# Kernel optimization log

Hardware: AMD Instinct MI355X
Metric: run time of the kernel (lower is better)

Reference implementation:

```python
import jax, jax.numpy as jnp
import numpy as np

PC = (-51.2, -51.2, -5.0, 51.2, 51.2, 3.0)
BEV_H, BEV_W, BEV_Z = 50, 50, 4
NCAM, NUM_HEADS = 6, 8
EPS = 1e-5


def _layer_norm(x, g, b):
    m = jnp.mean(x, -1, keepdims=True)
    v = jnp.mean((x - m) ** 2, -1, keepdims=True)
    return (x - m) / jnp.sqrt(v + 1e-5) * g + b


def _grid_sample(imgs, pts):
    # imgs: (B,C,H,W); pts: (B,N,2) normalized coords; bilinear,
    # align_corners=False, zero padding (matches F.grid_sample defaults).
    B, C, H, W = imgs.shape
    def one(img, p):
        x = ((p[:, 0] + 1.0) * W - 1.0) * 0.5
        y = ((p[:, 1] + 1.0) * H - 1.0) * 0.5
        x0 = jnp.floor(x); y0 = jnp.floor(y)
        wx = x - x0; wy = y - y0
        def g(xi, yi):
            ok = (xi >= 0) & (xi < W) & (yi >= 0) & (yi < H)
            v = img[:, jnp.clip(yi, 0, H - 1).astype(jnp.int32),
                       jnp.clip(xi, 0, W - 1).astype(jnp.int32)]
            return v * ok[None, :]
        return (g(x0, y0) * (1 - wx) * (1 - wy) + g(x0 + 1, y0) * wx * (1 - wy)
                + g(x0, y0 + 1) * (1 - wx) * wy + g(x0 + 1, y0 + 1) * wx * wy)
    return jax.vmap(one)(imgs, pts)  # (B,C,N)


def _mha(q, kv, inW, inb, outW, outb):
    # torch nn.MultiheadAttention (batch_first)
    C = q.shape[-1]; d = C // NUM_HEADS
    B, Nq = q.shape[:2]; Nk = kv.shape[1]
    Q = q @ inW[:C].T + inb[:C]
    K = kv @ inW[C:2 * C].T + inb[C:2 * C]
    V = kv @ inW[2 * C:].T + inb[2 * C:]
    Qh = Q.reshape(B, Nq, NUM_HEADS, d).transpose(0, 2, 1, 3)
    Kh = K.reshape(B, Nk, NUM_HEADS, d).transpose(0, 2, 1, 3)
    Vh = V.reshape(B, Nk, NUM_HEADS, d).transpose(0, 2, 1, 3)
    s = jnp.einsum('bhqd,bhkd->bhqk', Qh, Kh) / float(np.sqrt(d))
    a = jax.nn.softmax(s, axis=-1)
    o = jnp.einsum('bhqk,bhkd->bhqd', a, Vh).transpose(0, 2, 1, 3).reshape(B, Nq, C)
    return o @ outW.T + outb


def _warp_prev(prev_bev, ego_motion):
    B, N, C = prev_bev.shape
    sp = prev_bev.transpose(0, 2, 1).reshape(B, C, BEV_H, BEV_W)
    tx = ego_motion[:, 0, 3]; ty = ego_motion[:, 1, 3]
    yaw = jnp.arctan2(ego_motion[:, 1, 0], ego_motion[:, 0, 0])
    dx = tx / ((PC[3] - PC[0]) / BEV_W) * 2.0 / BEV_W
    dy = ty / ((PC[4] - PC[1]) / BEV_H) * 2.0 / BEV_H
    c = jnp.cos(yaw); s = jnp.sin(yaw)
    theta = jnp.stack([jnp.stack([c, -s, dx], -1),
                       jnp.stack([s, c, dy], -1)], axis=1)  # (B,2,3)
    # F.affine_grid, align_corners=False: output-pixel-center base grid
    xs = (2.0 * jnp.arange(BEV_W) + 1.0) / BEV_W - 1.0
    ys = (2.0 * jnp.arange(BEV_H) + 1.0) / BEV_H - 1.0
    gx, gy = jnp.meshgrid(xs, ys)  # (H,W) each
    base = jnp.stack([gx, gy, jnp.ones_like(gx)], -1)  # (H,W,3)
    grid = jnp.einsum('bij,hwj->bhwi', theta, base).reshape(B, -1, 2)
    out = _grid_sample(sp, grid)  # (B,C,N)
    return out.transpose(0, 2, 1)


def _reference_points(B):
    ys = (jnp.arange(BEV_H, dtype=jnp.float32) + 0.5) / BEV_H
    xs = (jnp.arange(BEV_W, dtype=jnp.float32) + 0.5) / BEV_W
    ry, rx = jnp.meshgrid(ys, xs, indexing='ij')
    rx = rx.reshape(-1); ry = ry.reshape(-1)
    zs = (jnp.arange(BEV_Z, dtype=jnp.float32) + 0.5) / BEV_Z
    N = BEV_H * BEV_W
    ref = jnp.stack([jnp.broadcast_to(rx[:, None], (N, BEV_Z)),
                     jnp.broadcast_to(ry[:, None], (N, BEV_Z)),
                     jnp.broadcast_to(zs[None, :], (N, BEV_Z))], -1)
    return jnp.broadcast_to(ref[None], (B, N, BEV_Z, 3))  # (B,Nq,Z,3)


def _point_sampling(ref, img_feats, lidar2img):
    B, Nq, Zb, _ = ref.shape
    _, Ncam, C, Hf, Wf = img_feats.shape
    x = ref[..., 0] * (PC[3] - PC[0]) + PC[0]
    y = ref[..., 1] * (PC[4] - PC[1]) + PC[1]
    z = ref[..., 2] * (PC[5] - PC[2]) + PC[2]
    pts = jnp.stack([x, y, z, jnp.ones_like(x)], -1).reshape(B, 1, Nq * Zb, 4)
    pts = jnp.broadcast_to(pts, (B, Ncam, Nq * Zb, 4))
    cam = jnp.einsum('bnij,bnpj->bnpi', lidar2img, pts)
    depth = cam[..., 2]
    xy = cam[..., 0:2] / jnp.clip(depth, EPS)[..., None]
    gx = (xy[..., 0] / (Wf - 1) - 0.5) * 2.0
    gy = (xy[..., 1] / (Hf - 1) - 0.5) * 2.0
    valid = ((depth > EPS) & (gx > -1.0) & (gx < 1.0)
             & (gy > -1.0) & (gy < 1.0))  # (B,Ncam,Nq*Zb)
    grid = jnp.stack([gx, gy], -1).reshape(B * Ncam, Nq * Zb, 2)
    samp = _grid_sample(img_feats.reshape(B * Ncam, C, Hf, Wf), grid)
    samp = samp.reshape(B, Ncam, C, Nq, Zb) * valid.reshape(B, Ncam, 1, Nq, Zb)
    return jnp.nan_to_num(samp)


def _forward(query, prev_bev, img_feats, ego_motion, lidar2img,
             attn_w_W, attn_w_b, sca_out_W, sca_out_b,
             in_proj_W, in_proj_b, mha_out_W, mha_out_b,
             norm1_g, norm1_b, ffn_W1, ffn_b1, ffn_W2, ffn_b2,
             norm2_g, norm2_b):
    B, Nq, C = query.shape
    # Temporal self-attention with warped previous BEV
    aligned = _warp_prev(prev_bev, ego_motion)
    kv = jnp.concatenate([query, aligned], axis=1)
    attn = _mha(query, kv, in_proj_W, in_proj_b, mha_out_W, mha_out_b)
    q = _layer_norm(query + attn, norm1_g, norm1_b)
    # Spatial cross attention
    ref = _reference_points(B)
    samp = _point_sampling(ref, img_feats, lidar2img)  # (B,Ncam,C,Nq,Z)
    w = (q @ attn_w_W.T + attn_w_b).reshape(B, Nq, NCAM * BEV_Z)
    w = jax.nn.softmax(w, axis=-1).reshape(B, Nq, NCAM, BEV_Z)
    agg = jnp.einsum('bncqz,bqnz->bqc', samp, w)
    q = agg @ sca_out_W.T + sca_out_b + q
    # FFN (Linear -> ReLU -> Linear -> LayerNorm), residual outside
    h = jax.nn.relu(q @ ffn_W1.T + ffn_b1) @ ffn_W2.T + ffn_b2
    return q + _layer_norm(h, norm2_g, norm2_b)


def setup_inputs() -> dict:
    key = jax.random.key(0)
    ks = jax.random.split(key, 16)
    B, Nq, C, Hf, Wf = 1, BEV_H * BEV_W, 256, 28, 50
    s = 0.02
    d = {
        'query': jax.random.normal(ks[0], (B, Nq, C), jnp.float32),
        'prev_bev': jax.random.normal(ks[1], (B, Nq, C), jnp.float32),
        'img_feats': jax.random.normal(ks[2], (B, NCAM, C, Hf, Wf), jnp.float32),
        'ego_motion': jax.random.normal(ks[3], (B, 4, 4), jnp.float32),
        'lidar2img': jax.random.normal(ks[4], (B, NCAM, 4, 4), jnp.float32),
        'attn_w_W': jax.random.normal(ks[5], (NCAM * BEV_Z, C), jnp.float32) * s,
        'attn_w_b': jnp.zeros((NCAM * BEV_Z,), jnp.float32),
        'sca_out_W': jax.random.normal(ks[6], (C, C), jnp.float32) * s,
        'sca_out_b': jnp.zeros((C,), jnp.float32),
        'in_proj_W': jax.random.normal(ks[7], (3 * C, C), jnp.float32) * s,
        'in_proj_b': jnp.zeros((3 * C,), jnp.float32),
        'mha_out_W': jax.random.normal(ks[8], (C, C), jnp.float32) * s,
        'mha_out_b': jnp.zeros((C,), jnp.float32),
        'norm1_g': jnp.ones((C,), jnp.float32),
        'norm1_b': jnp.zeros((C,), jnp.float32),
        'ffn_W1': jax.random.normal(ks[9], (2 * C, C), jnp.float32) * s,
        'ffn_b1': jnp.zeros((2 * C,), jnp.float32),
        'ffn_W2': jax.random.normal(ks[10], (C, 2 * C), jnp.float32) * s,
        'ffn_b2': jnp.zeros((C,), jnp.float32),
        'norm2_g': jnp.ones((C,), jnp.float32),
        'norm2_b': jnp.zeros((C,), jnp.float32),
    }
    return d


def reference(query, prev_bev, img_feats, ego_motion, lidar2img,
              attn_w_W, attn_w_b, sca_out_W, sca_out_b,
              in_proj_W, in_proj_b, mha_out_W, mha_out_b,
              norm1_g, norm1_b, ffn_W1, ffn_b1, ffn_W2, ffn_b2,
              norm2_g, norm2_b):
    return _forward(query, prev_bev, img_feats, ego_motion, lidar2img,
                    attn_w_W, attn_w_b, sca_out_W, sca_out_b,
                    in_proj_W, in_proj_b, mha_out_W, mha_out_b,
                    norm1_g, norm1_b, ffn_W1, ffn_b1, ffn_W2, ffn_b2,
                    norm2_g, norm2_b)
```

## Files before the change

### kernel.cpp

```cpp
#include <hip/hip_runtime.h>
#include <hip/hip_bf16.h>
#include <math.h>

#define NQ   2500
#define CDIM 256
#define NKV  5000
#define NH   8
#define DH   32
#define SPLITS 10
#define KPS   500
#define FULLT 7
#define TAILNK 52

typedef __attribute__((ext_vector_type(8))) short bf16x8;
typedef __attribute__((ext_vector_type(4))) short short4v;
typedef __attribute__((ext_vector_type(4))) float f32x4;

#define MFMA __builtin_amdgcn_mfma_f32_16x16x32_bf16

__device__ __forceinline__ short f2bf(float f) {
  union { float f; unsigned u; } v; v.f = f;
  unsigned r = v.u + 0x7FFFu + ((v.u >> 16) & 1u);
  return (short)(r >> 16);
}
__device__ __forceinline__ float bf2f(unsigned short s) {
  union { unsigned u; float f; } x; x.u = ((unsigned)s) << 16; return x.f;
}
__device__ __forceinline__ unsigned pk_trunc(float a, float b) {
  union { float f; unsigned u; } x, y; x.f = a; y.f = b;
  return (y.u & 0xFFFF0000u) | (x.u >> 16);
}
__device__ __forceinline__ unsigned cvt_pk_bf16(float a, float b) {
  unsigned r;
  asm("v_cvt_pk_bf16_f32 %0, %1, %2" : "=v"(r) : "v"(a), "v"(b));
  return r;
}
__device__ __forceinline__ float exp2_fast(float x) {
  float r; asm("v_exp_f32 %0, %1" : "=v"(r) : "v"(x)); return r;
}
__device__ __forceinline__ bf16x8 cat4(short4v a, short4v b) {
  bf16x8 r;
  r[0]=a[0]; r[1]=a[1]; r[2]=a[2]; r[3]=a[3];
  r[4]=b[0]; r[5]=b[1]; r[6]=b[2]; r[7]=b[3];
  return r;
}

__global__ __launch_bounds__(256) void k_build_kv(
    const float* __restrict__ query, const float* __restrict__ prev,
    const float* __restrict__ ego, float* __restrict__ kv)
{
  int row = blockIdx.x, c = threadIdx.x;
  if (row < NQ) { kv[(size_t)row*CDIM + c] = query[(size_t)row*CDIM + c]; return; }
  int n = row - NQ;
  float txm = ego[3], tym = ego[7];
  float yaw = atan2f(ego[4], ego[0]);
  float cs = cosf(yaw), sn = sinf(yaw);
  float dx = txm * (1.f/51.2f), dy = tym * (1.f/51.2f);
  int i = n / 50, j = n % 50;
  float gx = (2.f*j + 1.f)*(1.f/50.f) - 1.f;
  float gy = (2.f*i + 1.f)*(1.f/50.f) - 1.f;
  float px = cs*gx - sn*gy + dx;
  float py = sn*gx + cs*gy + dy;
  float xf = ((px + 1.f)*50.f - 1.f)*0.5f;
  float yf = ((py + 1.f)*50.f - 1.f)*0.5f;
  float x0f = floorf(xf), y0f = floorf(yf);
  int x0 = (int)x0f, y0 = (int)y0f;
  float wx = xf - x0f, wy = yf - y0f;
  float v00 = (x0  >=0 && x0  <50 && y0  >=0 && y0  <50) ? prev[((size_t)(y0*50+x0      ))*CDIM + c] : 0.f;
  float v10 = (x0+1>=0 && x0+1<50 && y0  >=0 && y0  <50) ? prev[((size_t)(y0*50+x0+1    ))*CDIM + c] : 0.f;
  float v01 = (x0  >=0 && x0  <50 && y0+1>=0 && y0+1<50) ? prev[((size_t)((y0+1)*50+x0  ))*CDIM + c] : 0.f;
  float v11 = (x0+1>=0 && x0+1<50 && y0+1>=0 && y0+1<50) ? prev[((size_t)((y0+1)*50+x0+1))*CDIM + c] : 0.f;
  float v = (v00*(1.f-wx) + v10*wx)*(1.f-wy) + (v01*(1.f-wx) + v11*wx)*wy;
  kv[(size_t)row*CDIM + c] = v;
}

__global__ __launch_bounds__(256) void k_transpose_img(
    const float* __restrict__ img, unsigned short* __restrict__ imgT)
{
  int b = blockIdx.x;
  int n = b / 28, y = b % 28;
  int c = threadIdx.x;
  for (int x = 0; x < 50; ++x)
    imgT[((size_t)((n*28 + y)*50 + x))*CDIM + c] =
      (unsigned short)f2bf(img[((size_t)(n*CDIM + c)*28 + y)*50 + x]);
}

__global__ __launch_bounds__(256) void k_gemm(
    const float* __restrict__ A, const float* __restrict__ W,
    const float* __restrict__ bias, const float* __restrict__ res,
    float* __restrict__ C, short* __restrict__ Cb,
    int M, int N, int K, int relu, int mode, float scale)
{
  __shared__ short Abf[8][33][8];
  __shared__ short Wbf[8][65][8];
  const int tid = threadIdx.x;
  const int lane = tid & 63, wid = tid >> 6;
  const int wm = wid >> 1, wn = wid & 1;
  const int g = lane >> 4, c = lane & 15;
  const int m0 = blockIdx.y << 5, n0 = blockIdx.x << 6;
  const int srow = tid >> 3, skq = tid & 7;
  f32x4 acc0 = {0.f,0.f,0.f,0.f}, acc1 = acc0;
  const float4 z4 = make_float4(0.f,0.f,0.f,0.f);
  for (int k0 = 0; k0 < K; k0 += 64) {
    float4 fa0 = z4, fa1 = z4;
    if (m0 + srow < M) {
      const float* ap = A + (size_t)(m0+srow)*K + k0 + skq*8;
      fa0 = *(const float4*)ap; fa1 = *(const float4*)(ap+4);
    }
    const float* wp0 = W + (size_t)(n0+srow)*K + k0 + skq*8;
    const float* wp1 = W + (size_t)(n0+32+srow)*K + k0 + skq*8;
    const float4 fw00 = *(const float4*)wp0, fw01 = *(const float4*)(wp0+4);
    const float4 fw10 = *(const float4*)wp1, fw11 = *(const float4*)(wp1+4);
    __syncthreads();
    union { unsigned u[4]; bf16x8 v; } pa, pw0, pw1;
    pa.u[0]  = cvt_pk_bf16(fa0.x, fa0.y);  pa.u[1]  = cvt_pk_bf16(fa0.z, fa0.w);
    pa.u[2]  = cvt_pk_bf16(fa1.x, fa1.y);  pa.u[3]  = cvt_pk_bf16(fa1.z, fa1.w);
    pw0.u[0] = cvt_pk_bf16(fw00.x, fw00.y); pw0.u[1] = cvt_pk_bf16(fw00.z, fw00.w);
    pw0.u[2] = cvt_pk_bf16(fw01.x, fw01.y); pw0.u[3] = cvt_pk_bf16(fw01.z, fw01.w);
    pw1.u[0] = cvt_pk_bf16(fw10.x, fw10.y); pw1.u[1] = cvt_pk_bf16(fw10.z, fw10.w);
    pw1.u[2] = cvt_pk_bf16(fw11.x, fw11.y); pw1.u[3] = cvt_pk_bf16(fw11.z, fw11.w);
    *(bf16x8*)&Abf[skq][srow][0]      = pa.v;
    *(bf16x8*)&Wbf[skq][srow][0]      = pw0.v;
    *(bf16x8*)&Wbf[skq][32+srow][0]   = pw1.v;
    __syncthreads();
    #pragma unroll
    for (int s = 0; s < 2; ++s) {
      const bf16x8 fA  = *(const bf16x8*)&Abf[s*4+g][wm*16 + c][0];
      const bf16x8 fW0 = *(const bf16x8*)&Wbf[s*4+g][wn*32 + c][0];
      const bf16x8 fW1 = *(const bf16x8*)&Wbf[s*4+g][wn*32 + 16 + c][0];
      acc0 = MFMA(fA, fW0, acc0, 0,0,0);
      acc1 = MFMA(fA, fW1, acc1, 0,0,0);
    }
  }
  const int nc0 = n0 + wn*32 + c, nc1 = nc0 + 16;
  const float b0v = bias[nc0], b1v = bias[nc1];
  #pragma unroll
  for (int r = 0; r < 4; ++r) {
    const int m = m0 + wm*16 + g*4 + r;
    if (m >= M) continue;
    float v0 = acc0[r] + b0v;
    float v1 = acc1[r] + b1v;
    if (mode == 0) {
      if (res) { v0 += res[(size_t)m*N + nc0]; v1 += res[(size_t)m*N + nc1]; }
      if (relu) { v0 = fmaxf(v0, 0.f); v1 = fmaxf(v1, 0.f); }
      C[(size_t)m*N + nc0] = v0;
      C[(size_t)m*N + nc1] = v1;
    } else if (mode == 1) {
      Cb[(size_t)m*N + nc0] = f2bf(v0*scale);
      Cb[(size_t)m*N + nc1] = f2bf(v1*scale);
    } else {
      Cb[(size_t)nc0*M + m] = f2bf(v0);
      Cb[(size_t)nc1*M + m] = f2bf(v1);
    }
  }
}

__device__ __forceinline__ void softmax_pv(
    f32x4 s0, f32x4 s1, f32x4 s2, f32x4 s3, bool tail, int g,
    float& m, float& l, f32x4& oA, f32x4& oB,
    bf16x8 A0lo, bf16x8 A0hi, bf16x8 A1lo, bf16x8 A1hi)
{
  float sv[16];
  #pragma unroll
  for (int r=0;r<4;++r){ sv[r]=s0[r]; sv[4+r]=s1[r]; sv[8+r]=s2[r]; sv[12+r]=s3[r]; }
  if (tail) {
    #pragma unroll
    for (int i=0;i<16;++i) {
      const int kl = (i>>2)*16 + g*4 + (i&3);
      if (kl >= TAILNK) sv[i] = -1e30f;
    }
  }
  float mx = fmaxf(fmaxf(fmaxf(sv[0],sv[1]),fmaxf(sv[2],sv[3])),
                   fmaxf(fmaxf(sv[4],sv[5]),fmaxf(sv[6],sv[7])));
  mx = fmaxf(mx, fmaxf(fmaxf(fmaxf(sv[8],sv[9]),fmaxf(sv[10],sv[11])),
                       fmaxf(fmaxf(sv[12],sv[13]),fmaxf(sv[14],sv[15]))));
  if (!__all(mx <= m + 8.f)) {
    float mm = fmaxf(mx, __shfl_xor(mx, 16));
    mm = fmaxf(mm, __shfl_xor(mm, 32));
    const float mn = fmaxf(m, mm);
    const float scl = exp2_fast(m - mn);
    m = mn;
    l *= scl;
    #pragma unroll
    for (int r=0;r<4;++r){ oA[r]*=scl; oB[r]*=scl; }
  }
  float p[16]; float ps = 0.f;
  #pragma unroll
  for (int i=0;i<16;++i){ p[i] = exp2_fast(sv[i]-m); ps += p[i]; }
  l += ps;
  union { unsigned u[4]; bf16x8 v; } b0, b1;
  #pragma unroll
  for (int i=0;i<4;++i) {
    b0.u[i] = pk_trunc(p[2*i],   p[2*i+1]);
    b1.u[i] = pk_trunc(p[8+2*i], p[8+2*i+1]);
  }
  oA = MFMA(A0lo, b0.v, oA, 0,0,0);
  oA = MFMA(A0hi, b1.v, oA, 0,0,0);
  oB = MFMA(A1lo, b0.v, oB, 0,0,0);
  oB = MFMA(A1hi, b1.v, oB, 0,0,0);
}

__global__ __launch_bounds__(64) void k_flash4(
    const short* __restrict__ Qbf, const short* __restrict__ Kbf,
    const short* __restrict__ VbfT, short* __restrict__ opart,
    float* __restrict__ mlp)
{
  const int lane = threadIdx.x;
  const int g = lane >> 4, c = lane & 15;
  const int h = blockIdx.y, sp = blockIdx.z;
  const int q0 = blockIdx.x * 32;
  const int qa  = min(q0 +      c, NQ-1);
  const int qb2 = min(q0 + 16 + c, NQ-1);
  const bf16x8 qf0 = *(const bf16x8*)(Qbf + (size_t)qa *CDIM + h*DH + g*8);
  const bf16x8 qf1 = *(const bf16x8*)(Qbf + (size_t)qb2*CDIM + h*DH + g*8);
  const int kbase = sp*KPS;
  const size_t doff = (size_t)h*DH + g*8;
  const short* kbp = Kbf + (size_t)(kbase + c)*CDIM + doff;
  const short* vr0 = VbfT + (size_t)(h*DH +      c)*NKV + kbase;
  const short* vr1 = VbfT + (size_t)(h*DH + 16 + c)*NKV + kbase;
  const f32x4 z = {0.f,0.f,0.f,0.f};
  f32x4 o00 = z, o01 = z, o10 = z, o11 = z;
  float m0v = -INFINITY, l0 = 0.f, m1v = -INFINITY, l1 = 0.f;

  bf16x8 kc0 = *(const bf16x8*)(kbp);
  bf16x8 kc1 = *(const bf16x8*)(kbp + (size_t)16*CDIM);
  bf16x8 kc2 = *(const bf16x8*)(kbp + (size_t)32*CDIM);
  bf16x8 kc3 = *(const bf16x8*)(kbp + (size_t)48*CDIM);

  #pragma unroll
  for (int t = 0; t < FULLT; ++t) {
    const int kt = t*64;
    const f32x4 s00 = MFMA(kc0, qf0, z, 0,0,0);
    const f32x4 s01 = MFMA(kc1, qf0, z, 0,0,0);
    const f32x4 s02 = MFMA(kc2, qf0, z, 0,0,0);
    const f32x4 s03 = MFMA(kc3, qf0, z, 0,0,0);
    const f32x4 s10 = MFMA(kc0, qf1, z, 0,0,0);
    const f32x4 s11 = MFMA(kc1, qf1, z, 0,0,0);
    const f32x4 s12 = MFMA(kc2, qf1, z, 0,0,0);
    const f32x4 s13 = MFMA(kc3, qf1, z, 0,0,0);
    if (t+1 < FULLT) {
      kc0 = *(const bf16x8*)(kbp + (size_t)(kt+64)*CDIM);
      kc1 = *(const bf16x8*)(kbp + (size_t)(kt+80)*CDIM);
      kc2 = *(const bf16x8*)(kbp + (size_t)(kt+96)*CDIM);
      kc3 = *(const bf16x8*)(kbp + (size_t)(kt+112)*CDIM);
    }
    const short4v x00 = *(const short4v*)(vr0 + kt      + g*4);
    const short4v x01 = *(const short4v*)(vr0 + kt + 16 + g*4);
    const short4v x02 = *(const short4v*)(vr0 + kt + 32 + g*4);
    const short4v x03 = *(const short4v*)(vr0 + kt + 48 + g*4);
    const short4v x10 = *(const short4v*)(vr1 + kt      + g*4);
    const short4v x11 = *(const short4v*)(vr1 + kt + 16 + g*4);
    const short4v x12 = *(const short4v*)(vr1 + kt + 32 + g*4);
    const short4v x13 = *(const short4v*)(vr1 + kt + 48 + g*4);
    const bf16x8 A0lo = cat4(x00, x01), A0hi = cat4(x02, x03);
    const bf16x8 A1lo = cat4(x10, x11), A1hi = cat4(x12, x13);
    softmax_pv(s00,s01,s02,s03, false, g, m0v, l0, o00, o01, A0lo, A0hi, A1lo, A1hi);
    softmax_pv(s10,s11,s12,s13, false, g, m1v, l1, o10, o11, A0lo, A0hi, A1lo, A1hi);
  }
  {
    const int kt = FULLT*64;
    const int ka0 = min(kbase + kt +      c, NKV-1);
    const int ka1 = min(kbase + kt + 16 + c, NKV-1);
    const int ka2 = min(kbase + kt + 32 + c, NKV-1);
    const int ka3 = min(kbase + kt + 48 + c, NKV-1);
    const bf16x8 kf0 = *(const bf16x8*)(Kbf + (size_t)ka0*CDIM + doff);
    const bf16x8 kf1 = *(const bf16x8*)(Kbf + (size_t)ka1*CDIM + doff);
    const bf16x8 kf2 = *(const bf16x8*)(Kbf + (size_t)ka2*CDIM + doff);
    const bf16x8 kf3 = *(const bf16x8*)(Kbf + (size_t)ka3*CDIM + doff);
    const f32x4 s00 = MFMA(kf0, qf0, z, 0,0,0);
    const f32x4 s01 = MFMA(kf1, qf0, z, 0,0,0);
    const f32x4 s02 = MFMA(kf2, qf0, z, 0,0,0);
    const f32x4 s03 = MFMA(kf3, qf0, z, 0,0,0);
    const f32x4 s10 = MFMA(kf0, qf1, z, 0,0,0);
    const f32x4 s11 = MFMA(kf1, qf1, z, 0,0,0);
    const f32x4 s12 = MFMA(kf2, qf1, z, 0,0,0);
    const f32x4 s13 = MFMA(kf3, qf1, z, 0,0,0);
    const int o0 = min(kt      + g*4, KPS-4);
    const int o1 = min(kt + 16 + g*4, KPS-4);
    const int o2 = min(kt + 32 + g*4, KPS-4);
    const int o3 = min(kt + 48 + g*4, KPS-4);
    const short4v x00 = *(const short4v*)(vr0 + o0);
    const short4v x01 = *(const short4v*)(vr0 + o1);
    const short4v x02 = *(const short4v*)(vr0 + o2);
    const short4v x03 = *(const short4v*)(vr0 + o3);
    const short4v x10 = *(const short4v*)(vr1 + o0);
    const short4v x11 = *(const short4v*)(vr1 + o1);
    const short4v x12 = *(const short4v*)(vr1 + o2);
    const short4v x13 = *(const short4v*)(vr1 + o3);
    const bf16x8 A0lo = cat4(x00, x01), A0hi = cat4(x02, x03);
    const bf16x8 A1lo = cat4(x10, x11), A1hi = cat4(x12, x13);
    softmax_pv(s00,s01,s02,s03, true, g, m0v, l0, o00, o01, A0lo, A0hi, A1lo, A1hi);
    softmax_pv(s10,s11,s12,s13, true, g, m1v, l1, o10, o11, A0lo, A0hi, A1lo, A1hi);
  }
  l0 += __shfl_xor(l0, 16); l0 += __shfl_xor(l0, 32);
  l1 += __shfl_xor(l1, 16); l1 += __shfl_xor(l1, 32);

  const size_t ob0 = (size_t)(sp*NH + h)*NQ;
  const int qw0 = q0 + c;
  if (qw0 < NQ) {
    const size_t b = (ob0 + qw0)*DH;
    #pragma unroll
    for (int r=0;r<4;++r) {
      opart[b +      g*4 + r] = f2bf(o00[r]);
      opart[b + 16 + g*4 + r] = f2bf(o01[r]);
    }
    if (g == 0) { mlp[(ob0 + qw0)*2] = m0v; mlp[(ob0 + qw0)*2+1] = l0; }
  }
  const int qw1 = q0 + 16 + c;
  if (qw1 < NQ) {
    const size_t b = (ob0 + qw1)*DH;
    #pragma unroll
    for (int r=0;r<4;++r) {
      opart[b +      g*4 + r] = f2bf(o10[r]);
      opart[b + 16 + g*4 + r] = f2bf(o11[r]);
    }
    if (g == 0) { mlp[(ob0 + qw1)*2] = m1v; mlp[(ob0 + qw1)*2+1] = l1; }
  }
}

__global__ __launch_bounds__(256) void k_combine(
    const short* __restrict__ opart, const float* __restrict__ mlp,
    float* __restrict__ attn)
{
  const int q = blockIdx.x, t = threadIdx.x;
  const int h = t >> 5, d = t & 31;
  float ms[SPLITS], ls[SPLITS];
  float mstar = -INFINITY;
  #pragma unroll
  for (int s = 0; s < SPLITS; ++s) {
    size_t b = (size_t)(s*NH + h)*NQ + q;
    ms[s] = mlp[b*2]; ls[s] = mlp[b*2+1];
    mstar = fmaxf(mstar, ms[s]);
  }
  float num = 0.f, den = 0.f;
  #pragma unroll
  for (int s = 0; s < SPLITS; ++s) {
    float e = exp2_fast(ms[s] - mstar);
    size_t b = (size_t)(s*NH + h)*NQ + q;
    num += bf2f((unsigned short)opart[b*DH + d])*e;
    den += ls[s]*e;
  }
  attn[(size_t)q*CDIM + t] = num/den;
}

__global__ __launch_bounds__(256) void k_ln(
    const float* __restrict__ x, const float* __restrict__ g,
    const float* __restrict__ b, const float* __restrict__ post_res,
    float* __restrict__ out)
{
  const int row = blockIdx.x, c = threadIdx.x;
  const size_t idx = (size_t)row*CDIM + c;
  const float v = x[idx];
  __shared__ float red[4];
  float s = v;
  #pragma unroll
  for (int m = 1; m < 64; m <<= 1) s += __shfl_xor(s, m);
  if ((c & 63) == 0) red[c >> 6] = s;
  __syncthreads();
  const float mean = (red[0]+red[1]+red[2]+red[3]) * (1.f/256.f);
  const float dv = v - mean;
  __syncthreads();
  float s2 = dv*dv;
  #pragma unroll
  for (int m = 1; m < 64; m <<= 1) s2 += __shfl_xor(s2, m);
  if ((c & 63) == 0) red[c >> 6] = s2;
  __syncthreads();
  const float var = (red[0]+red[1]+red[2]+red[3]) * (1.f/256.f);
  float o = dv * rsqrtf(var + 1e-5f) * g[c] + b[c];
  if (post_res) o += post_res[idx];
  out[idx] = o;
}

__global__ __launch_bounds__(256) void k_sample_agg(
    const float* __restrict__ q1, const unsigned short* __restrict__ imgT,
    const float* __restrict__ l2i, const float* __restrict__ awW,
    const float* __restrict__ awb, float* __restrict__ agg)
{
  const int q = blockIdx.x, tid = threadIdx.x;
  __shared__ float qrow[256];
  __shared__ float wl[24];
  __shared__ float fwx[24], fwy[24];
  __shared__ int iv[24], ix[24], iy[24];
  qrow[tid] = q1[(size_t)q*CDIM + tid];
  __syncthreads();
  if (tid < 192) {
    const int e = tid >> 3, s2 = tid & 7;
    float acc = 0.f;
    for (int c = s2; c < 256; c += 8) acc += qrow[c]*awW[e*256 + c];
    acc += __shfl_xor(acc,1);
    acc += __shfl_xor(acc,2);
    acc += __shfl_xor(acc,4);
    if (s2 == 0) wl[e] = acc + awb[e];
  }
  if (tid < 24) {
    const int e = tid, n = e >> 2, z = e & 3;
    const int iyq = q / 50, jxq = q % 50;
    const float rx = (jxq + 0.5f)*(1.f/50.f);
    const float ry = (iyq + 0.5f)*(1.f/50.f);
    const float rz = (z + 0.5f)*0.25f;
    const float X = rx*102.4f - 51.2f;
    const float Y = ry*102.4f - 51.2f;
    const float Z = rz*8.f - 5.f;
    const float* L = l2i + n*16;
    const float cx = L[0]*X + L[1]*Y + L[2]*Z  + L[3];
    const float cy = L[4]*X + L[5]*Y + L[6]*Z  + L[7];
    const float cd = L[8]*X + L[9]*Y + L[10]*Z + L[11];
    const float dn = fmaxf(cd, 1e-5f);
    const float u = cx/dn, vv = cy/dn;
    const float gx = (u*(1.f/49.f) - 0.5f)*2.f;
    const float gy = (vv*(1.f/27.f) - 0.5f)*2.f;
    const int ok = (cd > 1e-5f) && (gx > -1.f) && (gx < 1.f) && (gy > -1.f) && (gy < 1.f);
    const float xf = ((gx + 1.f)*50.f - 1.f)*0.5f;
    const float yf = ((gy + 1.f)*28.f - 1.f)*0.5f;
    const float x0f = floorf(xf), y0f = floorf(yf);
    iv[e] = ok; ix[e] = (int)x0f; iy[e] = (int)y0f;
    fwx[e] = xf - x0f; fwy[e] = yf - y0f;
  }
  __syncthreads();
  float mx = -INFINITY;
  #pragma unroll
  for (int e = 0; e < 24; ++e) mx = fmaxf(mx, wl[e]);
  float se = 0.f;
  #pragma unroll
  for (int e = 0; e < 24; ++e) se += __expf(wl[e]-mx);
  const float inv = 1.f/se;
  const int c = tid;
  float acc = 0.f;
  #pragma unroll
  for (int e = 0; e < 24; ++e) {
    if (!iv[e]) continue;
    const float w = __expf(wl[e]-mx)*inv;
    const int n = e >> 2;
    const int x0 = ix[e], y0 = iy[e];
    const float wx = fwx[e], wy = fwy[e];
    const size_t base = (size_t)(n*28)*50;
    float v00 = (x0  >=0 && x0  <50 && y0  >=0 && y0  <28) ? bf2f(imgT[((base + (size_t)y0*50     + x0  ))*CDIM + c]) : 0.f;
    float v10 = (x0+1>=0 && x0+1<50 && y0  >=0 && y0  <28) ? bf2f(imgT[((base + (size_t)y0*50     + x0+1))*CDIM + c]) : 0.f;
    float v01 = (x0  >=0 && x0  <50 && y0+1>=0 && y0+1<28) ? bf2f(imgT[((base + (size_t)(y0+1)*50 + x0  ))*CDIM + c]) : 0.f;
    float v11 = (x0+1>=0 && x0+1<50 && y0+1>=0 && y0+1<28) ? bf2f(imgT[((base + (size_t)(y0+1)*50 + x0+1))*CDIM + c]) : 0.f;
    acc += w * ((v00*(1.f-wx) + v10*wx)*(1.f-wy) + (v01*(1.f-wx) + v11*wx)*wy);
  }
  agg[(size_t)q*CDIM + c] = acc;
}

extern "C" void kernel_launch(void* const* d_in, const int* in_sizes, int n_in,
                              void* d_out, int out_size, void* d_ws, size_t ws_size,
                              hipStream_t stream)
{
  const float* query = (const float*)d_in[0];
  const float* prev  = (const float*)d_in[1];
  const float* img   = (const float*)d_in[2];
  const float* ego   = (const float*)d_in[3];
  const float* l2i   = (const float*)d_in[4];
  const float* awW   = (const float*)d_in[5];
  const float* awb   = (const float*)d_in[6];
  const float* scaW  = (const float*)d_in[7];
  const float* scab  = (const float*)d_in[8];
  const float* inW   = (const float*)d_in[9];
  const float* inb   = (const float*)d_in[10];
  const float* moW   = (const float*)d_in[11];
  const float* mob   = (const float*)d_in[12];
  const float* n1g   = (const float*)d_in[13];
  const float* n1b   = (const float*)d_in[14];
  const float* fW1   = (const float*)d_in[15];
  const float* fb1   = (const float*)d_in[16];
  const float* fW2   = (const float*)d_in[17];
  const float* fb2   = (const float*)d_in[18];
  const float* n2g   = (const float*)d_in[19];
  const float* n2b   = (const float*)d_in[20];
  float* out = (float*)d_out;
  float* ws  = (float*)d_ws;

  float* kv    = ws;
  short* Qbf   = (short*)(ws + 1280000);
  short* Kbf   = (short*)(ws + 1600000);
  short* VbfT  = (short*)(ws + 2240000);
  short* opart = (short*)(ws + 2880000);
  float* mlp   = ws + 6080000;
  unsigned short* imgT = (unsigned short*)(ws + 6480000);
  float* attn  = ws;
  float* tmp1  = ws +  640000;
  float* q1    = ws + 1280000;
  float* aggb  = ws + 1920000;
  float* q2    = ws + 2560000;
  float* hbuf  = ws + 3200000;
  float* h2    = ws + 4480000;

  const float qscale = 0.2550727452794943f;

  k_build_kv<<<NKV, 256, 0, stream>>>(query, prev, ego, kv);
  k_transpose_img<<<6*28, 256, 0, stream>>>(img, imgT);
  k_gemm<<<dim3(4,79),  256, 0, stream>>>(kv, inW,          inb,     nullptr, nullptr, Qbf,  NQ,  256, 256, 0, 1, qscale);
  k_gemm<<<dim3(4,157), 256, 0, stream>>>(kv, inW + 65536,  inb+256, nullptr, nullptr, Kbf,  NKV, 256, 256, 0, 1, 1.0f);
  k_gemm<<<dim3(4,157), 256, 0, stream>>>(kv, inW + 131072, inb+512, nullptr, nullptr, VbfT, NKV, 256, 256, 0, 2, 1.0f);
  k_flash4<<<dim3(79, NH, SPLITS), 64, 0, stream>>>(Qbf, Kbf, VbfT, opart, mlp);
  k_combine<<<NQ, 256, 0, stream>>>(opart, mlp, attn);
  k_gemm<<<dim3(4,79), 256, 0, stream>>>(attn, moW, mob, query, tmp1, nullptr, NQ, 256, 256, 0, 0, 1.0f);
  k_ln<<<NQ, 256, 0, stream>>>(tmp1, n1g, n1b, nullptr, q1);
  k_sample_agg<<<NQ, 256, 0, stream>>>(q1, imgT, l2i, awW, awb, aggb);
  k_gemm<<<dim3(4,79), 256, 0, stream>>>(aggb, scaW, scab, q1, q2, nullptr, NQ, 256, 256, 0, 0, 1.0f);
  k_gemm<<<dim3(8,79), 256, 0, stream>>>(q2, fW1, fb1, nullptr, hbuf, nullptr, NQ, 512, 256, 1, 0, 1.0f);
  k_gemm<<<dim3(4,79), 256, 0, stream>>>(hbuf, fW2, fb2, nullptr, h2, nullptr, NQ, 256, 512, 0, 0, 1.0f);
  k_ln<<<NQ, 256, 0, stream>>>(h2, n2g, n2b, q2, out);
}
```

Baseline: 149.7 us.

## Prepack weights and V into MFMA fragment layout, flatten flash grid

Adds a per-call kernel that converts all projection and FFN weights to bf16 in MFMA fragment order, so the GEMM reads B fragments straight from global memory instead of converting and staging them through shared memory. Adds a repack kernel that rearranges V into per-tile fragment order, letting the flash kernel load each operand with one 16-byte load instead of gathering short4 pieces. The flash grid is flattened so that heads and splits of the same query block are launched next to each other. Two extra launches and more workspace traffic are the price.

```diff
diff --git a/kernel.cpp b/kernel.cpp
--- a/kernel.cpp
+++ b/kernel.cpp
@@ -10,6 +10,7 @@
 #define SPLITS 10
 #define KPS   500
 #define FULLT 7
+#define TILES 8
 #define TAILNK 52
 
 typedef __attribute__((ext_vector_type(8))) short bf16x8;
@@ -37,12 +38,6 @@
 }
 __device__ __forceinline__ float exp2_fast(float x) {
   float r; asm("v_exp_f32 %0, %1" : "=v"(r) : "v"(x)); return r;
-}
-__device__ __forceinline__ bf16x8 cat4(short4v a, short4v b) {
-  bf16x8 r;
-  r[0]=a[0]; r[1]=a[1]; r[2]=a[2]; r[3]=a[3];
-  r[4]=b[0]; r[5]=b[1]; r[6]=b[2]; r[7]=b[3];
-  return r;
 }
 
 __global__ __launch_bounds__(256) void k_build_kv(
@@ -74,6 +69,51 @@
   kv[(size_t)row*CDIM + c] = v;
 }
 
+__global__ __launch_bounds__(256) void k_prep_w(
+    const float* __restrict__ inW, const float* __restrict__ moW,
+    const float* __restrict__ scaW, const float* __restrict__ fW1,
+    const float* __restrict__ fW2, short* __restrict__ wf)
+{
+  const int id = blockIdx.x*256 + threadIdx.x;
+  if (id >= 73728) return;
+  const int s = id*8;
+  const float* src; int off, K, obase;
+  if      (s < 65536)  { src = inW;          off = s;          K = 256; obase = 0; }
+  else if (s < 131072) { src = inW + 65536;  off = s - 65536;  K = 256; obase = 65536; }
+  else if (s < 196608) { src = inW + 131072; off = s - 131072; K = 256; obase = 131072; }
+  else if (s < 262144) { src = moW;          off = s - 196608; K = 256; obase = 196608; }
+  else if (s < 327680) { src = scaW;         off = s - 262144; K = 256; obase = 262144; }
+  else if (s < 458752) { src = fW1;          off = s - 327680; K = 256; obase = 327680; }
+  else                 { src = fW2;          off = s - 458752; K = 512; obase = 458752; }
+  const int n = off / K, k = off - n*K;
+  short4v lo, hi;
+  #pragma unroll
+  for (int j = 0; j < 4; ++j) { lo[j] = f2bf(src[off+j]); hi[j] = f2bf(src[off+4+j]); }
+  short* dst = wf + obase + (size_t)((n>>4)*(K>>3) + (k>>3))*128 + (n&15)*8;
+  *(short4v*)dst = lo;
+  *(short4v*)(dst+4) = hi;
+}
+
+__global__ __launch_bounds__(256) void k_repack_v(
+    const short* __restrict__ VbfT, short* __restrict__ Vf)
+{
+  const int idx = blockIdx.x*256 + threadIdx.x;
+  const int j    = idx & 7;
+  const int lane = (idx >> 3) & 63;
+  const int i    = (idx >> 9) & 1;
+  const int kt2  = (idx >> 10) & 1;
+  const int t    = (idx >> 11) & 7;
+  const int h    = (idx >> 14) & 7;
+  const int sp   = idx >> 17;
+  const int gg = lane >> 4, cc = lane & 15;
+  const int ko32 = ((j >> 2) << 4) | (gg << 2) | (j & 3);
+  const int kin = t*64 + kt2*32 + ko32;
+  const int d = i*16 + cc;
+  short v = 0;
+  if (kin < KPS) v = VbfT[(size_t)(h*32 + d)*NKV + sp*KPS + kin];
+  Vf[idx] = v;
+}
+
 __global__ __launch_bounds__(256) void k_transpose_img(
     const float* __restrict__ img, unsigned short* __restrict__ imgT)
 {
@@ -86,19 +126,21 @@
 }
 
 __global__ __launch_bounds__(256) void k_gemm(
-    const float* __restrict__ A, const float* __restrict__ W,
+    const float* __restrict__ A, const short* __restrict__ Wf,
     const float* __restrict__ bias, const float* __restrict__ res,
     float* __restrict__ C, short* __restrict__ Cb,
     int M, int N, int K, int relu, int mode, float scale)
 {
   __shared__ short Abf[8][33][8];
-  __shared__ short Wbf[8][65][8];
   const int tid = threadIdx.x;
   const int lane = tid & 63, wid = tid >> 6;
   const int wm = wid >> 1, wn = wid & 1;
   const int g = lane >> 4, c = lane & 15;
   const int m0 = blockIdx.y << 5, n0 = blockIdx.x << 6;
   const int srow = tid >> 3, skq = tid & 7;
+  const int kb8 = K >> 3;
+  const short* wfa = Wf + (size_t)((n0 + wn*32) >> 4)      * kb8 * 128 + c*8;
+  const short* wfb = Wf + (size_t)(((n0 + wn*32) >> 4) + 1) * kb8 * 128 + c*8;
   f32x4 acc0 = {0.f,0.f,0.f,0.f}, acc1 = acc0;
   const float4 z4 = make_float4(0.f,0.f,0.f,0.f);
   for (int k0 = 0; k0 < K; k0 += 64) {
@@ -107,27 +149,18 @@
       const float* ap = A + (size_t)(m0+srow)*K + k0 + skq*8;
       fa0 = *(const float4*)ap; fa1 = *(const float4*)(ap+4);
     }
-    const float* wp0 = W + (size_t)(n0+srow)*K + k0 + skq*8;
-    const float* wp1 = W + (size_t)(n0+32+srow)*K + k0 + skq*8;
-    const float4 fw00 = *(const float4*)wp0, fw01 = *(const float4*)(wp0+4);
-    const float4 fw10 = *(const float4*)wp1, fw11 = *(const float4*)(wp1+4);
     __syncthreads();
-    union { unsigned u[4]; bf16x8 v; } pa, pw0, pw1;
-    pa.u[0]  = cvt_pk_bf16(fa0.x, fa0.y);  pa.u[1]  = cvt_pk_bf16(fa0.z, fa0.w);
-    pa.u[2]  = cvt_pk_bf16(fa1.x, fa1.y);  pa.u[3]  = cvt_pk_bf16(fa1.z, fa1.w);
-    pw0.u[0] = cvt_pk_bf16(fw00.x, fw00.y); pw0.u[1] = cvt_pk_bf16(fw00.z, fw00.w);
-    pw0.u[2] = cvt_pk_bf16(fw01.x, fw01.y); pw0.u[3] = cvt_pk_bf16(fw01.z, fw01.w);
-    pw1.u[0] = cvt_pk_bf16(fw10.x, fw10.y); pw1.u[1] = cvt_pk_bf16(fw10.z, fw10.w);
-    pw1.u[2] = cvt_pk_bf16(fw11.x, fw11.y); pw1.u[3] = cvt_pk_bf16(fw11.z, fw11.w);
-    *(bf16x8*)&Abf[skq][srow][0]      = pa.v;
-    *(bf16x8*)&Wbf[skq][srow][0]      = pw0.v;
-    *(bf16x8*)&Wbf[skq][32+srow][0]   = pw1.v;
+    union { unsigned u[4]; bf16x8 v; } pa;
+    pa.u[0] = cvt_pk_bf16(fa0.x, fa0.y);  pa.u[1] = cvt_pk_bf16(fa0.z, fa0.w);
+    pa.u[2] = cvt_pk_bf16(fa1.x, fa1.y);  pa.u[3] = cvt_pk_bf16(fa1.z, fa1.w);
+    *(bf16x8*)&Abf[skq][srow][0] = pa.v;
     __syncthreads();
     #pragma unroll
     for (int s = 0; s < 2; ++s) {
+      const int kq = (k0 >> 3) + s*4 + g;
       const bf16x8 fA  = *(const bf16x8*)&Abf[s*4+g][wm*16 + c][0];
-      const bf16x8 fW0 = *(const bf16x8*)&Wbf[s*4+g][wn*32 + c][0];
-      const bf16x8 fW1 = *(const bf16x8*)&Wbf[s*4+g][wn*32 + 16 + c][0];
+      const bf16x8 fW0 = *(const bf16x8*)(wfa + (size_t)kq*128);
+      const bf16x8 fW1 = *(const bf16x8*)(wfb + (size_t)kq*128);
       acc0 = MFMA(fA, fW0, acc0, 0,0,0);
       acc1 = MFMA(fA, fW1, acc1, 0,0,0);
     }
@@ -200,15 +233,19 @@
   oB = MFMA(A1hi, b1.v, oB, 0,0,0);
 }
 
-__global__ __launch_bounds__(64) void k_flash4(
+__global__ __launch_bounds__(64) void k_flash5(
     const short* __restrict__ Qbf, const short* __restrict__ Kbf,
-    const short* __restrict__ VbfT, short* __restrict__ opart,
+    const short* __restrict__ Vf, short* __restrict__ opart,
     float* __restrict__ mlp)
 {
   const int lane = threadIdx.x;
   const int g = lane >> 4, c = lane & 15;
-  const int h = blockIdx.y, sp = blockIdx.z;
-  const int q0 = blockIdx.x * 32;
+  const int flat = blockIdx.x;
+  const int p  = flat % 80;
+  const int qb = flat / 80;
+  const int h  = p & 7;
+  const int sp = p >> 3;
+  const int q0 = qb * 32;
   const int qa  = min(q0 +      c, NQ-1);
   const int qb2 = min(q0 + 16 + c, NQ-1);
   const bf16x8 qf0 = *(const bf16x8*)(Qbf + (size_t)qa *CDIM + h*DH + g*8);
@@ -216,8 +253,7 @@
   const int kbase = sp*KPS;
   const size_t doff = (size_t)h*DH + g*8;
   const short* kbp = Kbf + (size_t)(kbase + c)*CDIM + doff;
-  const short* vr0 = VbfT + (size_t)(h*DH +      c)*NKV + kbase;
-  const short* vr1 = VbfT + (size_t)(h*DH + 16 + c)*NKV + kbase;
+  const short* vfp = Vf + (size_t)(sp*NH + h)*(TILES*2048) + lane*8;
   const f32x4 z = {0.f,0.f,0.f,0.f};
   f32x4 o00 = z, o01 = z, o10 = z, o11 = z;
   float m0v = -INFINITY, l0 = 0.f, m1v = -INFINITY, l1 = 0.f;
@@ -244,16 +280,11 @@
       kc2 = *(const bf16x8*)(kbp + (size_t)(kt+96)*CDIM);
       kc3 = *(const bf16x8*)(kbp + (size_t)(kt+112)*CDIM);
     }
-    const short4v x00 = *(const short4v*)(vr0 + kt      + g*4);
-    const short4v x01 = *(const short4v*)(vr0 + kt + 16 + g*4);
-    const short4v x02 = *(const short4v*)(vr0 + kt + 32 + g*4);
-    const short4v x03 = *(const short4v*)(vr0 + kt + 48 + g*4);
-    const short4v x10 = *(const short4v*)(vr1 + kt      + g*4);
-    const short4v x11 = *(const short4v*)(vr1 + kt + 16 + g*4);
-    const short4v x12 = *(const short4v*)(vr1 + kt + 32 + g*4);
-    const short4v x13 = *(const short4v*)(vr1 + kt + 48 + g*4);
-    const bf16x8 A0lo = cat4(x00, x01), A0hi = cat4(x02, x03);
-    const bf16x8 A1lo = cat4(x10, x11), A1hi = cat4(x12, x13);
+    const short* vt = vfp + (size_t)t*2048;
+    const bf16x8 A0lo = *(const bf16x8*)(vt       );
+    const bf16x8 A1lo = *(const bf16x8*)(vt +  512);
+    const bf16x8 A0hi = *(const bf16x8*)(vt + 1024);
+    const bf16x8 A1hi = *(const bf16x8*)(vt + 1536);
     softmax_pv(s00,s01,s02,s03, false, g, m0v, l0, o00, o01, A0lo, A0hi, A1lo, A1hi);
     softmax_pv(s10,s11,s12,s13, false, g, m1v, l1, o10, o11, A0lo, A0hi, A1lo, A1hi);
   }
@@ -275,20 +306,11 @@
     const f32x4 s11 = MFMA(kf1, qf1, z, 0,0,0);
     const f32x4 s12 = MFMA(kf2, qf1, z, 0,0,0);
     const f32x4 s13 = MFMA(kf3, qf1, z, 0,0,0);
-    const int o0 = min(kt      + g*4, KPS-4);
-    const int o1 = min(kt + 16 + g*4, KPS-4);
-    const int o2 = min(kt + 32 + g*4, KPS-4);
-    const int o3 = min(kt + 48 + g*4, KPS-4);
-    const short4v x00 = *(const short4v*)(vr0 + o0);
-    const short4v x01 = *(const short4v*)(vr0 + o1);
-    const short4v x02 = *(const short4v*)(vr0 + o2);
-    const short4v x03 = *(const short4v*)(vr0 + o3);
-    const short4v x10 = *(const short4v*)(vr1 + o0);
-    const short4v x11 = *(const short4v*)(vr1 + o1);
-    const short4v x12 = *(const short4v*)(vr1 + o2);
-    const short4v x13 = *(const short4v*)(vr1 + o3);
-    const bf16x8 A0lo = cat4(x00, x01), A0hi = cat4(x02, x03);
-    const bf16x8 A1lo = cat4(x10, x11), A1hi = cat4(x12, x13);
+    const short* vt = vfp + (size_t)FULLT*2048;
+    const bf16x8 A0lo = *(const bf16x8*)(vt       );
+    const bf16x8 A1lo = *(const bf16x8*)(vt +  512);
+    const bf16x8 A0hi = *(const bf16x8*)(vt + 1024);
+    const bf16x8 A1hi = *(const bf16x8*)(vt + 1536);
     softmax_pv(s00,s01,s02,s03, true, g, m0v, l0, o00, o01, A0lo, A0hi, A1lo, A1hi);
     softmax_pv(s10,s11,s12,s13, true, g, m1v, l1, o10, o11, A0lo, A0hi, A1lo, A1hi);
   }
@@ -454,17 +476,12 @@
   const float* l2i   = (const float*)d_in[4];
   const float* awW   = (const float*)d_in[5];
   const float* awb   = (const float*)d_in[6];
-  const float* scaW  = (const float*)d_in[7];
   const float* scab  = (const float*)d_in[8];
-  const float* inW   = (const float*)d_in[9];
   const float* inb   = (const float*)d_in[10];
-  const float* moW   = (const float*)d_in[11];
   const float* mob   = (const float*)d_in[12];
   const float* n1g   = (const float*)d_in[13];
   const float* n1b   = (const float*)d_in[14];
-  const float* fW1   = (const float*)d_in[15];
   const float* fb1   = (const float*)d_in[16];
-  const float* fW2   = (const float*)d_in[17];
   const float* fb2   = (const float*)d_in[18];
   const float* n2g   = (const float*)d_in[19];
   const float* n2b   = (const float*)d_in[20];
@@ -475,9 +492,11 @@
   short* Qbf   = (short*)(ws + 1280000);
   short* Kbf   = (short*)(ws + 1600000);
   short* VbfT  = (short*)(ws + 2240000);
-  short* opart = (short*)(ws + 2880000);
-  float* mlp   = ws + 6080000;
-  unsigned short* imgT = (unsigned short*)(ws + 6480000);
+  short* Vf    = (short*)(ws + 2880000);
+  short* opart = (short*)(ws + 3535360);
+  float* mlp   = ws + 6735360;
+  short* wf    = (short*)(ws + 7135360);
+  unsigned short* imgT = (unsigned short*)(ws + 7430272);
   float* attn  = ws;
   float* tmp1  = ws +  640000;
   float* q1    = ws + 1280000;
@@ -489,17 +508,21 @@
   const float qscale = 0.2550727452794943f;
 
   k_build_kv<<<NKV, 256, 0, stream>>>(query, prev, ego, kv);
+  k_prep_w<<<288, 256, 0, stream>>>((const float*)d_in[9], (const float*)d_in[11],
+                                    (const float*)d_in[7], (const float*)d_in[15],
+                                    (const float*)d_in[17], wf);
   k_transpose_img<<<6*28, 256, 0, stream>>>(img, imgT);
-  k_gemm<<<dim3(4,79),  256, 0, stream>>>(kv, inW,          inb,     nullptr, nullptr, Qbf,  NQ,  256, 256, 0, 1, qscale);
-  k_gemm<<<dim3(4,157), 256, 0, stream>>>(kv, inW + 65536,  inb+256, nullptr, nullptr, Kbf,  NKV, 256, 256, 0, 1, 1.0f);
-  k_gemm<<<dim3(4,157), 256, 0, stream>>>(kv, inW + 131072, inb+512, nullptr, nullptr, VbfT, NKV, 256, 256, 0, 2, 1.0f);
-  k_flash4<<<dim3(79, NH, SPLITS), 64, 0, stream>>>(Qbf, Kbf, VbfT, opart, mlp);
+  k_gemm<<<dim3(4,79),  256, 0, stream>>>(kv, wf,          inb,     nullptr, nullptr, Qbf,  NQ,  256, 256, 0, 1, qscale);
+  k_gemm<<<dim3(4,157), 256, 0, stream>>>(kv, wf +  65536, inb+256, nullptr, nullptr, Kbf,  NKV, 256, 256, 0, 1, 1.0f);
+  k_gemm<<<dim3(4,157), 256, 0, stream>>>(kv, wf + 131072, inb+512, nullptr, nullptr, VbfT, NKV, 256, 256, 0, 2, 1.0f);
+  k_repack_v<<<5120, 256, 0, stream>>>(VbfT, Vf);
+  k_flash5<<<79*80, 64, 0, stream>>>(Qbf, Kbf, Vf, opart, mlp);
   k_combine<<<NQ, 256, 0, stream>>>(opart, mlp, attn);
-  k_gemm<<<dim3(4,79), 256, 0, stream>>>(attn, moW, mob, query, tmp1, nullptr, NQ, 256, 256, 0, 0, 1.0f);
+  k_gemm<<<dim3(4,79), 256, 0, stream>>>(attn, wf + 196608, mob, query, tmp1, nullptr, NQ, 256, 256, 0, 0, 1.0f);
   k_ln<<<NQ, 256, 0, stream>>>(tmp1, n1g, n1b, nullptr, q1);
   k_sample_agg<<<NQ, 256, 0, stream>>>(q1, imgT, l2i, awW, awb, aggb);
-  k_gemm<<<dim3(4,79), 256, 0, stream>>>(aggb, scaW, scab, q1, q2, nullptr, NQ, 256, 256, 0, 0, 1.0f);
-  k_gemm<<<dim3(8,79), 256, 0, stream>>>(q2, fW1, fb1, nullptr, hbuf, nullptr, NQ, 512, 256, 1, 0, 1.0f);
-  k_gemm<<<dim3(4,79), 256, 0, stream>>>(hbuf, fW2, fb2, nullptr, h2, nullptr, NQ, 256, 512, 0, 0, 1.0f);
+  k_gemm<<<dim3(4,79), 256, 0, stream>>>(aggb, wf + 262144, scab, q1, q2, nullptr, NQ, 256, 256, 0, 0, 1.0f);
+  k_gemm<<<dim3(8,79), 256, 0, stream>>>(q2, wf + 327680, fb1, nullptr, hbuf, nullptr, NQ, 512, 256, 1, 0, 1.0f);
+  k_gemm<<<dim3(4,79), 256, 0, stream>>>(hbuf, wf + 458752, fb2, nullptr, h2, nullptr, NQ, 256, 512, 0, 0, 1.0f);
   k_ln<<<NQ, 256, 0, stream>>>(h2, n2g, n2b, q2, out);
 }
```

After: 152.6 us. About the same (+2.0%).
